# Kernel optimization log

Hardware: AMD Instinct MI355X
Metric: run time of the kernel (lower is better)

Reference implementation:

```python
import jax, jax.numpy as jnp
import numpy as np

# --- static config (mirrors args) ---
FOV = 79.0
RES = 5                      # map_resolution (cm/cell)
MAP_SIZE_CM = 4800           # map_size_cm // global_downscaling
VR = 100                     # vision_range (cells)
CAM_H_CM = 88.0              # camera_height * 100
CAT_THR, EXP_THR, MAP_THR = 5.0, 1.0, 1.0
MAX_H = 72                   # int(360 / 5)
MIN_H = -8                   # int(-40 / 5)
DEG = 57.29577951308232


def _splat(feat, coords, dims):
    """Trilinear splat (scatter-add) of feat [F,N] at coords [3,N] in [-1,1] into grid dims, then round."""
    F_, N = feat.shape
    Mtot = dims[0] * dims[1] * dims[2]
    pos = [coords[d] * dims[d] / 2.0 + dims[d] / 2.0 for d in range(3)]
    flo = [jnp.floor(p) for p in pos]
    grid = jnp.zeros((F_, Mtot), jnp.float32)
    for c0 in (0, 1):
        for c1 in (0, 1):
            for c2 in (0, 1):
                idx = jnp.zeros((N,), jnp.float32)
                wts = jnp.ones((N,), jnp.float32)
                for d, off in enumerate((c0, c1, c2)):
                    p = flo[d] + off
                    safe = ((p > 0) & (p < dims[d])).astype(jnp.float32)
                    wts = wts * (1.0 - jnp.abs(pos[d] - p)) * safe
                    idx = idx * dims[d] + p * safe
                grid = grid.at[:, idx.astype(jnp.int32)].add(feat * wts[None, :])
    return jnp.round(grid).reshape(F_, dims[0], dims[1], dims[2])


def _affine_grid(theta, H, W):
    # align_corners=True base grid; theta [2,3] -> grid [H,W,2] (x,y)
    gx, gy = jnp.meshgrid(jnp.linspace(-1.0, 1.0, W), jnp.linspace(-1.0, 1.0, H))
    base = jnp.stack([gx, gy, jnp.ones_like(gx)], -1)  # [H,W,3]
    return base @ theta.T


def _grid_sample(img, grid):
    # bilinear, zero padding, align_corners=True. img [C,H,W], grid [H,W,2]
    C, H, W = img.shape
    x = (grid[..., 0] + 1.0) * 0.5 * (W - 1)
    y = (grid[..., 1] + 1.0) * 0.5 * (H - 1)
    x0 = jnp.floor(x); y0 = jnp.floor(y)
    out = jnp.zeros_like(img)
    for yy, xx in ((y0, x0), (y0, x0 + 1), (y0 + 1, x0), (y0 + 1, x0 + 1)):
        w = (1.0 - jnp.abs(x - xx)) * (1.0 - jnp.abs(y - yy))
        inb = ((xx >= 0) & (xx <= W - 1) & (yy >= 0) & (yy <= H - 1)).astype(img.dtype)
        xi = jnp.clip(xx, 0, W - 1).astype(jnp.int32)
        yi = jnp.clip(yy, 0, H - 1).astype(jnp.int32)
        out = out + img[:, yi, xi] * (w * inb)[None]
    return out


def _forward(obs, pose_obs, maps_last, poses_last):
    bs, c, h, w = obs.shape
    depth = obs[0, 3]  # [h,w] in cm
    # camera matrix
    xc = (w - 1.0) / 2.0
    zc = (h - 1.0) / 2.0
    f = (w / 2.0) / np.tan(np.deg2rad(FOV / 2.0))
    gx = jnp.arange(w, dtype=jnp.float32)[None, :]
    gz = jnp.arange(h - 1, -1, -1, dtype=jnp.float32)[:, None]
    X = (gx - xc) * depth / f
    Z = (gz - zc) * depth / f
    # camera->agent (elevation 0 -> identity rot) then shift_loc (theta=pi/2 -> identity rot)
    X = X + VR * RES // 2
    Z = Z + CAM_H_CM
    zdim = MAX_H - MIN_H
    xs = (X / RES - VR // 2.0) / VR * 2.0
    ys = (depth / RES - VR // 2.0) / VR * 2.0
    zs = (Z / RES - (MAX_H + MIN_H) // 2.0) / zdim * 2.0
    N = h * w
    coords = jnp.stack([xs.reshape(N), ys.reshape(N), zs.reshape(N)], 0)  # [3,N]
    feat = jnp.concatenate([jnp.ones((1, N), jnp.float32), obs[0, 4:].reshape(c - 4, N)], 0)  # [F,N]
    voxels = _splat(feat, coords, (VR, VR, zdim))       # [F,VR,VR,Z]
    voxels = jnp.swapaxes(voxels, 1, 2)                  # .transpose(2,3)
    min_z = int(25 / RES - MIN_H)                        # 13
    max_z = int((CAM_H_CM + 1) / RES - MIN_H)            # 25
    ahp = voxels[..., min_z:max_z].sum(-1)               # [F,VR,VR]
    allp = voxels.sum(-1)
    fp_map = jnp.clip(ahp[0:1] / MAP_THR, 0.0, 1.0)
    fp_exp = jnp.clip(allp[0:1] / EXP_THR, 0.0, 1.0)
    M = MAP_SIZE_CM // RES
    x1 = M // 2 - VR // 2; x2 = x1 + VR
    y1 = M // 2; y2 = y1 + VR
    agent_view = jnp.zeros((c, M, M), jnp.float32)
    agent_view = agent_view.at[0:1, y1:y2, x1:x2].set(fp_map)
    agent_view = agent_view.at[1:2, y1:y2, x1:x2].set(fp_exp)
    agent_view = agent_view.at[4:, y1:y2, x1:x2].set(jnp.clip(ahp[1:] / CAT_THR, 0.0, 1.0))
    # pose integration (note: pose_pred aliases poses_last which is updated in-place in torch)
    th = poses_last[2] / DEG
    ny = poses_last[1] + pose_obs[0] * jnp.sin(th) + pose_obs[1] * jnp.cos(th)
    nx = poses_last[0] + pose_obs[0] * jnp.cos(th) - pose_obs[1] * jnp.sin(th)
    nt = poses_last[2] + pose_obs[2] * DEG
    nt = jnp.fmod(nt - 180.0, 360.0) + 180.0
    nt = jnp.fmod(nt + 180.0, 360.0) - 180.0
    current_pose = jnp.stack([nx, ny, nt])
    # spatial transform (st_pose is detached in torch)
    st = jax.lax.stop_gradient(current_pose)
    half = M // 2
    sx = -(st[0] * 100.0 / RES - half) / half
    sy = -(st[1] * 100.0 / RES - half) / half
    sth = (90.0 - st[2]) * np.pi / 180.0
    ct, sn = jnp.cos(sth), jnp.sin(sth)
    z = jnp.zeros(()); o = jnp.ones(())
    theta1 = jnp.stack([jnp.stack([ct, -sn, z]), jnp.stack([sn, ct, z])])
    theta2 = jnp.stack([jnp.stack([o, z, sx]), jnp.stack([z, o, sy])])
    rotated = _grid_sample(agent_view, _affine_grid(theta1, M, M))
    translated = _grid_sample(rotated, _affine_grid(theta2, M, M))
    # snap positive semantic cells (channels 4..7) to per-channel feature max
    ks = feat[1:5].max(axis=1)  # [4]
    sem = translated[4:8]
    translated = translated.at[4:8].set(jnp.where(sem > 0.0, ks[:, None, None], sem))
    map_pred = jnp.maximum(maps_last, translated)
    return fp_map, map_pred, current_pose, current_pose


def setup_inputs() -> dict:
    key = jax.random.key(0)
    k1, k2, k3, k4 = jax.random.split(key, 4)
    C = 9
    obs = jax.random.uniform(k1, (1, C, 480, 640), dtype=jnp.float32)
    obs = obs.at[:, 3].set(obs[:, 3] * 400.0 + 50.0)  # depth in cm, 50..450
    pose_obs = jax.random.uniform(k2, (3,), dtype=jnp.float32) * jnp.array([0.2, 0.2, 0.1], jnp.float32)
    maps_last = jax.random.uniform(k3, (C, 960, 960), dtype=jnp.float32)
    poses_last = jnp.array([24.0, 24.0, 0.0], jnp.float32) + jax.random.uniform(k4, (3,), dtype=jnp.float32) * jnp.array([2.0, 2.0, 30.0], jnp.float32)
    return {"obs": obs, "pose_obs": pose_obs, "maps_last": maps_last, "poses_last": poses_last}


def reference(obs, pose_obs, maps_last, poses_last):
    return _forward(obs, pose_obs, maps_last, poses_last)
```

## Files before the change

### kernel.cpp

```cpp
#include <hip/hip_runtime.h>
#include <math.h>

#define NPIX (480*640)
#define MDIM 960
#define MPIX (MDIM*MDIM)

#define CNT_OFF   0
#define CUR_OFF   10000
#define SCAL_OFF  20000
#define MEMSET_U32 20016
#define OFFS_OFF  20016
#define SM_OFF    30024
#define PAY_OFF   100024

#define OUT_FPMAP 0
#define OUT_MAP   10000
#define OUT_POSE  (10000 + 9*MPIX)

__global__ void pose_kernel(const float* pose_obs, const float* poses_last,
                            float* scal, float* out_pose) {
    if (threadIdx.x == 0) {
        const float DEGc = 57.29577951308232f;
        float th = poses_last[2] / DEGc;
        float s = sinf(th), c = cosf(th);
        float ny = poses_last[1] + pose_obs[0]*s + pose_obs[1]*c;
        float nx = poses_last[0] + pose_obs[0]*c - pose_obs[1]*s;
        float nt = poses_last[2] + pose_obs[2]*DEGc;
        nt = fmodf(nt - 180.0f, 360.0f) + 180.0f;
        nt = fmodf(nt + 180.0f, 360.0f) - 180.0f;
        out_pose[0] = nx; out_pose[1] = ny; out_pose[2] = nt;
        out_pose[3] = nx; out_pose[4] = ny; out_pose[5] = nt;
        float sx = -((nx*100.0f)/5.0f - 480.0f)/480.0f;
        float sy = -((ny*100.0f)/5.0f - 480.0f)/480.0f;
        float sth = ((90.0f - nt) * 3.14159265358979323846f) / 180.0f;
        scal[0] = cosf(sth);
        scal[1] = sinf(sth);
        scal[2] = sx;
        scal[3] = sy;
    }
}

__global__ void ks_kernel(const float* __restrict__ obs, float* scal) {
    int tid = blockIdx.x*blockDim.x + threadIdx.x;
    int stride = gridDim.x*blockDim.x;
    float m0 = 0.0f, m1 = 0.0f, m2 = 0.0f, m3 = 0.0f;
    for (int p = tid; p < NPIX; p += stride) {
        m0 = fmaxf(m0, obs[4*NPIX + p]);
        m1 = fmaxf(m1, obs[5*NPIX + p]);
        m2 = fmaxf(m2, obs[6*NPIX + p]);
        m3 = fmaxf(m3, obs[7*NPIX + p]);
    }
    #pragma unroll
    for (int off = 32; off > 0; off >>= 1) {
        m0 = fmaxf(m0, __shfl_down(m0, off, 64));
        m1 = fmaxf(m1, __shfl_down(m1, off, 64));
        m2 = fmaxf(m2, __shfl_down(m2, off, 64));
        m3 = fmaxf(m3, __shfl_down(m3, off, 64));
    }
    if ((threadIdx.x & 63) == 0) {
        atomicMax((int*)&scal[4], __float_as_int(m0));
        atomicMax((int*)&scal[5], __float_as_int(m1));
        atomicMax((int*)&scal[6], __float_as_int(m2));
        atomicMax((int*)&scal[7], __float_as_int(m3));
    }
}

__device__ __forceinline__ void pix_pos(const float* __restrict__ obs, int pix, float fcam,
                                        float& pos0, float& pos1, float& pos2) {
    int i = pix / 640, j = pix - i*640;
    float d = obs[3*NPIX + pix];
    float X = ((float)j - 319.5f) * d / fcam + 250.0f;
    float Z = ((float)(479 - i) - 239.5f) * d / fcam + 88.0f;
    float xs = ((X/5.0f - 50.0f)/100.0f)*2.0f;
    float ys = ((d/5.0f - 50.0f)/100.0f)*2.0f;
    float zs = ((Z/5.0f - 32.0f)/80.0f)*2.0f;
    pos0 = (xs*100.0f)/2.0f + 50.0f;
    pos1 = (ys*100.0f)/2.0f + 50.0f;
    pos2 = (zs*80.0f)/2.0f + 40.0f;
}

__global__ __launch_bounds__(256) void count_kernel(const float* __restrict__ obs,
                                                    unsigned* __restrict__ cnt, float fcam) {
    int pix = blockIdx.x*blockDim.x + threadIdx.x;
    if (pix >= NPIX) return;
    float p0, p1, p2;
    pix_pos(obs, pix, fcam, p0, p1, p2);
    int bx = (int)floorf(p0), by = (int)floorf(p1), bz = (int)floorf(p2);
    if (bx < 0 || bx > 99 || by < 0 || by > 99 || bz < 0 || bz > 79) return;
    atomicAdd(&cnt[bx*100 + by], 1u);
}

__global__ __launch_bounds__(1024) void scan_kernel(const unsigned* __restrict__ cnt,
                                                    unsigned* __restrict__ offs) {
    __shared__ unsigned part[1024];
    int tid = threadIdx.x;
    int base = tid * 10;
    unsigned local[10];
    unsigned s = 0;
    #pragma unroll
    for (int q = 0; q < 10; q++) {
        unsigned v = (base + q < 10000) ? cnt[base + q] : 0u;
        local[q] = s;
        s += v;
    }
    part[tid] = s;
    __syncthreads();
    for (int off = 1; off < 1024; off <<= 1) {
        unsigned v = (tid >= off) ? part[tid - off] : 0u;
        __syncthreads();
        part[tid] += v;
        __syncthreads();
    }
    unsigned chunk_excl = (tid > 0) ? part[tid - 1] : 0u;
    #pragma unroll
    for (int q = 0; q < 10; q++) {
        if (base + q <= 10000) offs[base + q] = chunk_excl + local[q];
    }
}

__global__ __launch_bounds__(256) void scatter_kernel(const float* __restrict__ obs,
                                                      const unsigned* __restrict__ offs,
                                                      unsigned* __restrict__ cur,
                                                      float4* __restrict__ pay, float fcam) {
    int pix = blockIdx.x*blockDim.x + threadIdx.x;
    if (pix >= NPIX) return;
    float p0, p1, p2;
    pix_pos(obs, pix, fcam, p0, p1, p2);
    int bx = (int)floorf(p0), by = (int)floorf(p1), bz = (int)floorf(p2);
    if (bx < 0 || bx > 99 || by < 0 || by > 99 || bz < 0 || bz > 79) return;
    int b = bx*100 + by;
    unsigned slot = atomicAdd(&cur[b], 1u);
    unsigned k = offs[b] + slot;
    float f1 = obs[4*NPIX + pix];
    float f2 = obs[5*NPIX + pix];
    float f3 = obs[6*NPIX + pix];
    float f4 = obs[7*NPIX + pix];
    float f5 = obs[8*NPIX + pix];
    pay[2*k + 0] = make_float4(p0, p1, p2, f1);
    pay[2*k + 1] = make_float4(f2, f3, f4, f5);
}

__global__ __launch_bounds__(256) void gather_kernel(const float4* __restrict__ pay,
                                                     const unsigned* __restrict__ offs,
                                                     float* __restrict__ sm,
                                                     float* __restrict__ out_fp) {
    int t = blockIdx.x;
    int x = t % 100, y = t / 100;
    int tid = threadIdx.x;
    int sub = tid >> 6;
    int lane = tid & 63;
    __shared__ float zacc[80*6];
    for (int q = tid; q < 480; q += 256) zacc[q] = 0.0f;
    __syncthreads();
    if (x >= 1 && y >= 1) {
        int bx = x - 1 + (sub & 1);
        int by = y - 1 + (sub >> 1);
        int b = bx*100 + by;
        unsigned s = offs[b], e = offs[b+1];
        for (unsigned k = s + lane; k < e; k += 64) {
            float4 a  = pay[2*k + 0];
            float4 q2 = pay[2*k + 1];
            float w0 = 1.0f - fabsf(a.x - (float)x);
            float w1 = 1.0f - fabsf(a.y - (float)y);
            float w01 = w0 * w1;
            float bzf = floorf(a.z);
            #pragma unroll
            for (int c2 = 0; c2 <= 1; c2++) {
                float p2 = bzf + (float)c2;
                if (!(p2 > 0.0f && p2 < 80.0f)) continue;
                float w = w01 * (1.0f - fabsf(a.z - p2));
                int zb = (int)p2 * 6;
                atomicAdd(&zacc[zb + 0], w);
                atomicAdd(&zacc[zb + 1], w*a.w);
                atomicAdd(&zacc[zb + 2], w*q2.x);
                atomicAdd(&zacc[zb + 3], w*q2.y);
                atomicAdd(&zacc[zb + 4], w*q2.z);
                atomicAdd(&zacc[zb + 5], w*q2.w);
            }
        }
    }
    __syncthreads();
    if (tid < 64) {
        int z = lane;
        float r0 = rintf(zacc[z*6 + 0]);
        float all0 = r0;
        if (lane < 16) all0 += rintf(zacc[(z + 64)*6 + 0]);
        bool inb = (z >= 13 && z < 25);
        float a0 = inb ? r0 : 0.0f;
        float a1 = inb ? rintf(zacc[z*6 + 1]) : 0.0f;
        float a2 = inb ? rintf(zacc[z*6 + 2]) : 0.0f;
        float a3 = inb ? rintf(zacc[z*6 + 3]) : 0.0f;
        float a4 = inb ? rintf(zacc[z*6 + 4]) : 0.0f;
        float a5 = inb ? rintf(zacc[z*6 + 5]) : 0.0f;
        #pragma unroll
        for (int off = 32; off > 0; off >>= 1) {
            all0 += __shfl_down(all0, off, 64);
            a0 += __shfl_down(a0, off, 64);
            a1 += __shfl_down(a1, off, 64);
            a2 += __shfl_down(a2, off, 64);
            a3 += __shfl_down(a3, off, 64);
            a4 += __shfl_down(a4, off, 64);
            a5 += __shfl_down(a5, off, 64);
        }
        if (lane == 0) {
            float fp = fminf(a0, 1.0f);
            float ex = fminf(all0, 1.0f);
            sm[0*10000 + t] = fp;
            sm[1*10000 + t] = ex;
            sm[2*10000 + t] = fminf(a1/5.0f, 1.0f);
            sm[3*10000 + t] = fminf(a2/5.0f, 1.0f);
            sm[4*10000 + t] = fminf(a3/5.0f, 1.0f);
            sm[5*10000 + t] = fminf(a4/5.0f, 1.0f);
            sm[6*10000 + t] = fminf(a5/5.0f, 1.0f);
            out_fp[t] = fp;
        }
    }
}

__device__ __forceinline__ void sample_agent(float gxv, float gyv,
                                             float ct, float sn,
                                             const float* __restrict__ sm,
                                             float rot[7]) {
    float u = ct*gxv - sn*gyv;
    float v = sn*gxv + ct*gyv;
    float xim = ((u + 1.0f)*0.5f)*959.0f;
    float yim = ((v + 1.0f)*0.5f)*959.0f;
    float x0 = floorf(xim), y0 = floorf(yim);
    #pragma unroll
    for (int ty = 0; ty <= 1; ty++) {
        float yy = y0 + (float)ty;
        if (yy < 480.0f || yy >= 580.0f) continue;
        float wy = 1.0f - fabsf(yim - yy);
        int yi = (int)yy - 480;
        #pragma unroll
        for (int tx = 0; tx <= 1; tx++) {
            float xx = x0 + (float)tx;
            if (xx < 430.0f || xx >= 530.0f) continue;
            float w = (1.0f - fabsf(xim - xx)) * wy;
            int o = yi*100 + ((int)xx - 430);
            #pragma unroll
            for (int k = 0; k < 7; k++) rot[k] += sm[k*10000 + o] * w;
        }
    }
}

__global__ __launch_bounds__(256) void final_kernel(const float* __restrict__ maps_last,
                                                    const float* __restrict__ sm,
                                                    const float* __restrict__ scal,
                                                    float* __restrict__ out_map) {
    int t = blockIdx.x*blockDim.x + threadIdx.x;
    if (t >= MPIX) return;
    int y = t / MDIM, x = t - y*MDIM;
    float ct = scal[0], sn = scal[1], sx = scal[2], sy = scal[3];
    float ks0 = scal[4], ks1 = scal[5], ks2 = scal[6], ks3 = scal[7];
    const float step = 2.0f/959.0f;
    float gxv = (float)x*step - 1.0f;
    float gyv = (float)y*step - 1.0f;
    float u = gxv + sx, v = gyv + sy;
    float xim = ((u + 1.0f)*0.5f)*959.0f;
    float yim = ((v + 1.0f)*0.5f)*959.0f;
    float ts[7] = {0,0,0,0,0,0,0};

    float gxc = xim*step - 1.0f;
    float gyc = yim*step - 1.0f;
    float uc = ct*gxc - sn*gyc;
    float vc = sn*gxc + ct*gyc;
    float xc2 = ((uc + 1.0f)*0.5f)*959.0f;
    float yc2 = ((vc + 1.0f)*0.5f)*959.0f;
    bool active = (xc2 > 427.5f) && (xc2 < 531.5f) && (yc2 > 477.5f) && (yc2 < 581.5f);

    if (active) {
        float x0 = floorf(xim), y0 = floorf(yim);
        #pragma unroll
        for (int ty = 0; ty <= 1; ty++) {
            float yy = y0 + (float)ty;
            if (yy < 0.0f || yy > 959.0f) continue;
            float wy = 1.0f - fabsf(yim - yy);
            #pragma unroll
            for (int tx = 0; tx <= 1; tx++) {
                float xx = x0 + (float)tx;
                if (xx < 0.0f || xx > 959.0f) continue;
                float w = (1.0f - fabsf(xim - xx)) * wy;
                float rot[7] = {0,0,0,0,0,0,0};
                float gx1 = xx*step - 1.0f;
                float gy1 = yy*step - 1.0f;
                sample_agent(gx1, gy1, ct, sn, sm, rot);
                #pragma unroll
                for (int k = 0; k < 7; k++) ts[k] += rot[k]*w;
            }
        }
    }
    int o = t;
    float ml;
    ml = maps_last[0*MPIX + o]; out_map[0*MPIX + o] = fmaxf(ml, ts[0]);
    ml = maps_last[1*MPIX + o]; out_map[1*MPIX + o] = fmaxf(ml, ts[1]);
    ml = maps_last[2*MPIX + o]; out_map[2*MPIX + o] = fmaxf(ml, 0.0f);
    ml = maps_last[3*MPIX + o]; out_map[3*MPIX + o] = fmaxf(ml, 0.0f);
    float t4 = ts[2]; t4 = (t4 > 0.0f) ? ks0 : t4;
    ml = maps_last[4*MPIX + o]; out_map[4*MPIX + o] = fmaxf(ml, t4);
    float t5 = ts[3]; t5 = (t5 > 0.0f) ? ks1 : t5;
    ml = maps_last[5*MPIX + o]; out_map[5*MPIX + o] = fmaxf(ml, t5);
    float t6 = ts[4]; t6 = (t6 > 0.0f) ? ks2 : t6;
    ml = maps_last[6*MPIX + o]; out_map[6*MPIX + o] = fmaxf(ml, t6);
    float t7 = ts[5]; t7 = (t7 > 0.0f) ? ks3 : t7;
    ml = maps_last[7*MPIX + o]; out_map[7*MPIX + o] = fmaxf(ml, t7);
    ml = maps_last[8*MPIX + o]; out_map[8*MPIX + o] = fmaxf(ml, ts[6]);
}

extern "C" void kernel_launch(void* const* d_in, const int* in_sizes, int n_in,
                              void* d_out, int out_size, void* d_ws, size_t ws_size,
                              hipStream_t stream) {
    const float* obs        = (const float*)d_in[0];
    const float* pose_obs   = (const float*)d_in[1];
    const float* maps_last  = (const float*)d_in[2];
    const float* poses_last = (const float*)d_in[3];
    float* out = (float*)d_out;

    unsigned* ws_u = (unsigned*)d_ws;
    float*    ws_f = (float*)d_ws;
    unsigned* cnt  = ws_u + CNT_OFF;
    unsigned* cur  = ws_u + CUR_OFF;
    float*    scal = ws_f + SCAL_OFF;
    unsigned* offs = ws_u + OFFS_OFF;
    float*    sm   = ws_f + SM_OFF;
    float4*   pay  = (float4*)(ws_f + PAY_OFF);

    hipMemsetAsync(d_ws, 0, (size_t)MEMSET_U32 * 4, stream);

    float fcam = (float)(320.0 / tan(39.5 * M_PI / 180.0));

    pose_kernel<<<1, 64, 0, stream>>>(pose_obs, poses_last, scal, out + OUT_POSE);
    ks_kernel<<<128, 256, 0, stream>>>(obs, scal);
    count_kernel<<<(NPIX + 255)/256, 256, 0, stream>>>(obs, cnt, fcam);
    scan_kernel<<<1, 1024, 0, stream>>>(cnt, offs);
    scatter_kernel<<<(NPIX + 255)/256, 256, 0, stream>>>(obs, offs, cur, pay, fcam);
    gather_kernel<<<10000, 256, 0, stream>>>(pay, offs, sm, out + OUT_FPMAP);
    final_kernel<<<(MPIX + 255)/256, 256, 0, stream>>>(maps_last, sm, scal, out + OUT_MAP);
}
```

Before: 266.6 us.

## Fuse count/ks and scan/pose kernels, record ranks, vectorize pixel loops

Merges the depth-bin counting with the semantic-channel max reduction, and the prefix scan with the pose computation, which removes two launches. The count pass stores each pixel's bin and atomic rank so the scatter pass no longer needs a second atomic counter. Pixel and map kernels now process four elements per thread with float4 loads. The gather kernel assigns one wave per cell and reads two adjacent bins as a single contiguous range. The final kernel takes a fast path that streams maps_last through when none of a thread's four pixels fall in the agent window. This adds a packed-rank buffer and a wave-level scan; the ks reduction now starts from the first element rather than zero, which matches only if the feature values are nonnegative.

```diff
diff --git a/kernel.cpp b/kernel.cpp
--- a/kernel.cpp
+++ b/kernel.cpp
@@ -4,22 +4,105 @@
 #define NPIX (480*640)
 #define MDIM 960
 #define MPIX (MDIM*MDIM)
-
-#define CNT_OFF   0
-#define CUR_OFF   10000
-#define SCAL_OFF  20000
-#define MEMSET_U32 20016
-#define OFFS_OFF  20016
-#define SM_OFF    30024
-#define PAY_OFF   100024
+#define PACK_M 307201u
+
+#define CNT_OFF    0
+#define SCAL_OFF   10000
+#define MEMSET_U32 10016
+#define OFFS_OFF   10016
+#define SM_OFF     20024
+#define PACK_OFF   90024
+#define PAY_OFF    397224
 
 #define OUT_FPMAP 0
 #define OUT_MAP   10000
 #define OUT_POSE  (10000 + 9*MPIX)
 
-__global__ void pose_kernel(const float* pose_obs, const float* poses_last,
-                            float* scal, float* out_pose) {
-    if (threadIdx.x == 0) {
+__global__ __launch_bounds__(256) void count_ks_kernel(const float* __restrict__ obs,
+                                                       unsigned* __restrict__ cnt,
+                                                       unsigned* __restrict__ pack,
+                                                       float* scal, float fcam) {
+    int g = blockIdx.x*256 + threadIdx.x;
+    int p = g*4;
+    int i = p / 640, j0 = p - i*640;
+    float4 d4 = *(const float4*)(obs + 3*NPIX + p);
+    float dv[4] = {d4.x, d4.y, d4.z, d4.w};
+    #pragma unroll
+    for (int q = 0; q < 4; q++) {
+        float d = dv[q];
+        float X = ((float)(j0+q) - 319.5f) * d / fcam + 250.0f;
+        float Z = ((float)(479 - i) - 239.5f) * d / fcam + 88.0f;
+        float xs = ((X/5.0f - 50.0f)/100.0f)*2.0f;
+        float ys = ((d/5.0f - 50.0f)/100.0f)*2.0f;
+        float zs = ((Z/5.0f - 32.0f)/80.0f)*2.0f;
+        float pos0 = (xs*100.0f)/2.0f + 50.0f;
+        float pos1 = (ys*100.0f)/2.0f + 50.0f;
+        float pos2 = (zs*80.0f)/2.0f + 40.0f;
+        int bx = (int)floorf(pos0), by = (int)floorf(pos1), bz = (int)floorf(pos2);
+        unsigned pk = 0xFFFFFFFFu;
+        if (bx >= 0 && bx <= 99 && by >= 0 && by <= 99 && bz >= 0 && bz <= 79) {
+            unsigned b = (unsigned)(bx*100 + by);
+            unsigned rank = atomicAdd(&cnt[b], 1u);
+            pk = b * PACK_M + rank;
+        }
+        pack[p+q] = pk;
+    }
+    float4 a = *(const float4*)(obs + 4*NPIX + p);
+    float4 b4 = *(const float4*)(obs + 5*NPIX + p);
+    float4 c4 = *(const float4*)(obs + 6*NPIX + p);
+    float4 e4 = *(const float4*)(obs + 7*NPIX + p);
+    float m0 = fmaxf(fmaxf(a.x,a.y), fmaxf(a.z,a.w));
+    float m1 = fmaxf(fmaxf(b4.x,b4.y), fmaxf(b4.z,b4.w));
+    float m2 = fmaxf(fmaxf(c4.x,c4.y), fmaxf(c4.z,c4.w));
+    float m3 = fmaxf(fmaxf(e4.x,e4.y), fmaxf(e4.z,e4.w));
+    #pragma unroll
+    for (int off = 32; off > 0; off >>= 1) {
+        m0 = fmaxf(m0, __shfl_down(m0, off, 64));
+        m1 = fmaxf(m1, __shfl_down(m1, off, 64));
+        m2 = fmaxf(m2, __shfl_down(m2, off, 64));
+        m3 = fmaxf(m3, __shfl_down(m3, off, 64));
+    }
+    if ((threadIdx.x & 63) == 0) {
+        atomicMax((int*)&scal[4], __float_as_int(m0));
+        atomicMax((int*)&scal[5], __float_as_int(m1));
+        atomicMax((int*)&scal[6], __float_as_int(m2));
+        atomicMax((int*)&scal[7], __float_as_int(m3));
+    }
+}
+
+__global__ __launch_bounds__(256) void scan_pose_kernel(const unsigned* __restrict__ cnt,
+                                                        unsigned* __restrict__ offs,
+                                                        const float* pose_obs,
+                                                        const float* poses_last,
+                                                        float* scal, float* out_pose) {
+    int tid = threadIdx.x;
+    int lane = tid & 63, wave = tid >> 6;
+    unsigned sum = 0;
+    #pragma unroll 4
+    for (int q = 0; q < 40; q++) {
+        int idx = tid*40 + q;
+        if (idx < 10000) sum += cnt[idx];
+    }
+    unsigned incl = sum;
+    #pragma unroll
+    for (int off = 1; off < 64; off <<= 1) {
+        unsigned u = (unsigned)__shfl_up((int)incl, off, 64);
+        if (lane >= off) incl += u;
+    }
+    __shared__ unsigned wtot[4];
+    if (lane == 63) wtot[wave] = incl;
+    __syncthreads();
+    unsigned pre = 0;
+    for (int w = 0; w < wave; w++) pre += wtot[w];
+    unsigned excl = pre + incl - sum;
+    unsigned run = excl;
+    #pragma unroll 4
+    for (int q = 0; q < 40; q++) {
+        int idx = tid*40 + q;
+        if (idx < 10000) { offs[idx] = run; run += cnt[idx]; }
+    }
+    if (tid == 255) {
+        offs[10000] = excl;
         const float DEGc = 57.29577951308232f;
         float th = poses_last[2] / DEGc;
         float s = sinf(th), c = cosf(th);
@@ -40,180 +123,121 @@
     }
 }
 
-__global__ void ks_kernel(const float* __restrict__ obs, float* scal) {
-    int tid = blockIdx.x*blockDim.x + threadIdx.x;
-    int stride = gridDim.x*blockDim.x;
-    float m0 = 0.0f, m1 = 0.0f, m2 = 0.0f, m3 = 0.0f;
-    for (int p = tid; p < NPIX; p += stride) {
-        m0 = fmaxf(m0, obs[4*NPIX + p]);
-        m1 = fmaxf(m1, obs[5*NPIX + p]);
-        m2 = fmaxf(m2, obs[6*NPIX + p]);
-        m3 = fmaxf(m3, obs[7*NPIX + p]);
-    }
-    #pragma unroll
-    for (int off = 32; off > 0; off >>= 1) {
-        m0 = fmaxf(m0, __shfl_down(m0, off, 64));
-        m1 = fmaxf(m1, __shfl_down(m1, off, 64));
-        m2 = fmaxf(m2, __shfl_down(m2, off, 64));
-        m3 = fmaxf(m3, __shfl_down(m3, off, 64));
-    }
-    if ((threadIdx.x & 63) == 0) {
-        atomicMax((int*)&scal[4], __float_as_int(m0));
-        atomicMax((int*)&scal[5], __float_as_int(m1));
-        atomicMax((int*)&scal[6], __float_as_int(m2));
-        atomicMax((int*)&scal[7], __float_as_int(m3));
-    }
-}
-
-__device__ __forceinline__ void pix_pos(const float* __restrict__ obs, int pix, float fcam,
-                                        float& pos0, float& pos1, float& pos2) {
-    int i = pix / 640, j = pix - i*640;
-    float d = obs[3*NPIX + pix];
-    float X = ((float)j - 319.5f) * d / fcam + 250.0f;
-    float Z = ((float)(479 - i) - 239.5f) * d / fcam + 88.0f;
-    float xs = ((X/5.0f - 50.0f)/100.0f)*2.0f;
-    float ys = ((d/5.0f - 50.0f)/100.0f)*2.0f;
-    float zs = ((Z/5.0f - 32.0f)/80.0f)*2.0f;
-    pos0 = (xs*100.0f)/2.0f + 50.0f;
-    pos1 = (ys*100.0f)/2.0f + 50.0f;
-    pos2 = (zs*80.0f)/2.0f + 40.0f;
-}
-
-__global__ __launch_bounds__(256) void count_kernel(const float* __restrict__ obs,
-                                                    unsigned* __restrict__ cnt, float fcam) {
-    int pix = blockIdx.x*blockDim.x + threadIdx.x;
-    if (pix >= NPIX) return;
-    float p0, p1, p2;
-    pix_pos(obs, pix, fcam, p0, p1, p2);
-    int bx = (int)floorf(p0), by = (int)floorf(p1), bz = (int)floorf(p2);
-    if (bx < 0 || bx > 99 || by < 0 || by > 99 || bz < 0 || bz > 79) return;
-    atomicAdd(&cnt[bx*100 + by], 1u);
-}
-
-__global__ __launch_bounds__(1024) void scan_kernel(const unsigned* __restrict__ cnt,
-                                                    unsigned* __restrict__ offs) {
-    __shared__ unsigned part[1024];
-    int tid = threadIdx.x;
-    int base = tid * 10;
-    unsigned local[10];
-    unsigned s = 0;
-    #pragma unroll
-    for (int q = 0; q < 10; q++) {
-        unsigned v = (base + q < 10000) ? cnt[base + q] : 0u;
-        local[q] = s;
-        s += v;
-    }
-    part[tid] = s;
-    __syncthreads();
-    for (int off = 1; off < 1024; off <<= 1) {
-        unsigned v = (tid >= off) ? part[tid - off] : 0u;
-        __syncthreads();
-        part[tid] += v;
-        __syncthreads();
-    }
-    unsigned chunk_excl = (tid > 0) ? part[tid - 1] : 0u;
-    #pragma unroll
-    for (int q = 0; q < 10; q++) {
-        if (base + q <= 10000) offs[base + q] = chunk_excl + local[q];
-    }
-}
-
 __global__ __launch_bounds__(256) void scatter_kernel(const float* __restrict__ obs,
                                                       const unsigned* __restrict__ offs,
-                                                      unsigned* __restrict__ cur,
+                                                      const unsigned* __restrict__ pack,
                                                       float4* __restrict__ pay, float fcam) {
-    int pix = blockIdx.x*blockDim.x + threadIdx.x;
-    if (pix >= NPIX) return;
-    float p0, p1, p2;
-    pix_pos(obs, pix, fcam, p0, p1, p2);
-    int bx = (int)floorf(p0), by = (int)floorf(p1), bz = (int)floorf(p2);
-    if (bx < 0 || bx > 99 || by < 0 || by > 99 || bz < 0 || bz > 79) return;
-    int b = bx*100 + by;
-    unsigned slot = atomicAdd(&cur[b], 1u);
-    unsigned k = offs[b] + slot;
-    float f1 = obs[4*NPIX + pix];
-    float f2 = obs[5*NPIX + pix];
-    float f3 = obs[6*NPIX + pix];
-    float f4 = obs[7*NPIX + pix];
-    float f5 = obs[8*NPIX + pix];
-    pay[2*k + 0] = make_float4(p0, p1, p2, f1);
-    pay[2*k + 1] = make_float4(f2, f3, f4, f5);
-}
-
-__global__ __launch_bounds__(256) void gather_kernel(const float4* __restrict__ pay,
-                                                     const unsigned* __restrict__ offs,
-                                                     float* __restrict__ sm,
-                                                     float* __restrict__ out_fp) {
-    int t = blockIdx.x;
+    int g = blockIdx.x*256 + threadIdx.x;
+    int p = g*4;
+    int i = p / 640, j0 = p - i*640;
+    uint4 pk4 = *(const uint4*)(pack + p);
+    unsigned pks[4] = {pk4.x, pk4.y, pk4.z, pk4.w};
+    float4 d4 = *(const float4*)(obs + 3*NPIX + p);
+    float4 f14 = *(const float4*)(obs + 4*NPIX + p);
+    float4 f24 = *(const float4*)(obs + 5*NPIX + p);
+    float4 f34 = *(const float4*)(obs + 6*NPIX + p);
+    float4 f44 = *(const float4*)(obs + 7*NPIX + p);
+    float4 f54 = *(const float4*)(obs + 8*NPIX + p);
+    float dv[4] = {d4.x, d4.y, d4.z, d4.w};
+    float f1[4] = {f14.x, f14.y, f14.z, f14.w};
+    float f2[4] = {f24.x, f24.y, f24.z, f24.w};
+    float f3[4] = {f34.x, f34.y, f34.z, f34.w};
+    float f4v[4] = {f44.x, f44.y, f44.z, f44.w};
+    float f5[4] = {f54.x, f54.y, f54.z, f54.w};
+    #pragma unroll
+    for (int q = 0; q < 4; q++) {
+        unsigned pk = pks[q];
+        if (pk == 0xFFFFFFFFu) continue;
+        unsigned b = pk / PACK_M;
+        unsigned rank = pk - b * PACK_M;
+        unsigned k = offs[b] + rank;
+        float d = dv[q];
+        float X = ((float)(j0+q) - 319.5f) * d / fcam + 250.0f;
+        float Z = ((float)(479 - i) - 239.5f) * d / fcam + 88.0f;
+        float xs = ((X/5.0f - 50.0f)/100.0f)*2.0f;
+        float ys = ((d/5.0f - 50.0f)/100.0f)*2.0f;
+        float zs = ((Z/5.0f - 32.0f)/80.0f)*2.0f;
+        float pos0 = (xs*100.0f)/2.0f + 50.0f;
+        float pos1 = (ys*100.0f)/2.0f + 50.0f;
+        float pos2 = (zs*80.0f)/2.0f + 40.0f;
+        pay[2*k + 0] = make_float4(pos0, pos1, pos2, f1[q]);
+        pay[2*k + 1] = make_float4(f2[q], f3[q], f4v[q], f5[q]);
+    }
+}
+
+__global__ __launch_bounds__(1024) void gather_kernel(const float4* __restrict__ pay,
+                                                      const unsigned* __restrict__ offs,
+                                                      float* __restrict__ sm,
+                                                      float* __restrict__ out_fp) {
+    int wave = threadIdx.x >> 6, lane = threadIdx.x & 63;
+    int t = blockIdx.x*16 + wave;
     int x = t % 100, y = t / 100;
-    int tid = threadIdx.x;
-    int sub = tid >> 6;
-    int lane = tid & 63;
-    __shared__ float zacc[80*6];
-    for (int q = tid; q < 480; q += 256) zacc[q] = 0.0f;
+    __shared__ float zacc[16][480];
+    float* za = zacc[wave];
+    for (int q = lane; q < 480; q += 64) za[q] = 0.0f;
+    if (x >= 1 && y >= 1) {
+        int bb0 = (x-1)*100 + (y-1);
+        int bb1 = x*100 + (y-1);
+        #pragma unroll
+        for (int sgi = 0; sgi < 2; sgi++) {
+            int b = sgi ? bb1 : bb0;
+            unsigned s = offs[b], e = offs[b+2];
+            for (unsigned k = s + lane; k < e; k += 64) {
+                float4 a  = pay[2*k + 0];
+                float4 q2 = pay[2*k + 1];
+                float w0 = 1.0f - fabsf(a.x - (float)x);
+                float w1 = 1.0f - fabsf(a.y - (float)y);
+                float w01 = w0 * w1;
+                float bzf = floorf(a.z);
+                #pragma unroll
+                for (int c2 = 0; c2 <= 1; c2++) {
+                    float p2 = bzf + (float)c2;
+                    if (!(p2 > 0.0f && p2 < 80.0f)) continue;
+                    float w = w01 * (1.0f - fabsf(a.z - p2));
+                    int zb = (int)p2 * 6;
+                    atomicAdd(&za[zb + 0], w);
+                    atomicAdd(&za[zb + 1], w*a.w);
+                    atomicAdd(&za[zb + 2], w*q2.x);
+                    atomicAdd(&za[zb + 3], w*q2.y);
+                    atomicAdd(&za[zb + 4], w*q2.z);
+                    atomicAdd(&za[zb + 5], w*q2.w);
+                }
+            }
+        }
+    }
     __syncthreads();
-    if (x >= 1 && y >= 1) {
-        int bx = x - 1 + (sub & 1);
-        int by = y - 1 + (sub >> 1);
-        int b = bx*100 + by;
-        unsigned s = offs[b], e = offs[b+1];
-        for (unsigned k = s + lane; k < e; k += 64) {
-            float4 a  = pay[2*k + 0];
-            float4 q2 = pay[2*k + 1];
-            float w0 = 1.0f - fabsf(a.x - (float)x);
-            float w1 = 1.0f - fabsf(a.y - (float)y);
-            float w01 = w0 * w1;
-            float bzf = floorf(a.z);
-            #pragma unroll
-            for (int c2 = 0; c2 <= 1; c2++) {
-                float p2 = bzf + (float)c2;
-                if (!(p2 > 0.0f && p2 < 80.0f)) continue;
-                float w = w01 * (1.0f - fabsf(a.z - p2));
-                int zb = (int)p2 * 6;
-                atomicAdd(&zacc[zb + 0], w);
-                atomicAdd(&zacc[zb + 1], w*a.w);
-                atomicAdd(&zacc[zb + 2], w*q2.x);
-                atomicAdd(&zacc[zb + 3], w*q2.y);
-                atomicAdd(&zacc[zb + 4], w*q2.z);
-                atomicAdd(&zacc[zb + 5], w*q2.w);
-            }
-        }
-    }
-    __syncthreads();
-    if (tid < 64) {
-        int z = lane;
-        float r0 = rintf(zacc[z*6 + 0]);
-        float all0 = r0;
-        if (lane < 16) all0 += rintf(zacc[(z + 64)*6 + 0]);
-        bool inb = (z >= 13 && z < 25);
-        float a0 = inb ? r0 : 0.0f;
-        float a1 = inb ? rintf(zacc[z*6 + 1]) : 0.0f;
-        float a2 = inb ? rintf(zacc[z*6 + 2]) : 0.0f;
-        float a3 = inb ? rintf(zacc[z*6 + 3]) : 0.0f;
-        float a4 = inb ? rintf(zacc[z*6 + 4]) : 0.0f;
-        float a5 = inb ? rintf(zacc[z*6 + 5]) : 0.0f;
-        #pragma unroll
-        for (int off = 32; off > 0; off >>= 1) {
-            all0 += __shfl_down(all0, off, 64);
-            a0 += __shfl_down(a0, off, 64);
-            a1 += __shfl_down(a1, off, 64);
-            a2 += __shfl_down(a2, off, 64);
-            a3 += __shfl_down(a3, off, 64);
-            a4 += __shfl_down(a4, off, 64);
-            a5 += __shfl_down(a5, off, 64);
-        }
-        if (lane == 0) {
-            float fp = fminf(a0, 1.0f);
-            float ex = fminf(all0, 1.0f);
-            sm[0*10000 + t] = fp;
-            sm[1*10000 + t] = ex;
-            sm[2*10000 + t] = fminf(a1/5.0f, 1.0f);
-            sm[3*10000 + t] = fminf(a2/5.0f, 1.0f);
-            sm[4*10000 + t] = fminf(a3/5.0f, 1.0f);
-            sm[5*10000 + t] = fminf(a4/5.0f, 1.0f);
-            sm[6*10000 + t] = fminf(a5/5.0f, 1.0f);
-            out_fp[t] = fp;
-        }
+    int z = lane;
+    float r0 = rintf(za[z*6 + 0]);
+    float all0 = r0;
+    if (lane < 16) all0 += rintf(za[(z + 64)*6 + 0]);
+    bool inb = (z >= 13 && z < 25);
+    float a0 = inb ? r0 : 0.0f;
+    float a1 = inb ? rintf(za[z*6 + 1]) : 0.0f;
+    float a2 = inb ? rintf(za[z*6 + 2]) : 0.0f;
+    float a3 = inb ? rintf(za[z*6 + 3]) : 0.0f;
+    float a4 = inb ? rintf(za[z*6 + 4]) : 0.0f;
+    float a5 = inb ? rintf(za[z*6 + 5]) : 0.0f;
+    #pragma unroll
+    for (int off = 32; off > 0; off >>= 1) {
+        all0 += __shfl_down(all0, off, 64);
+        a0 += __shfl_down(a0, off, 64);
+        a1 += __shfl_down(a1, off, 64);
+        a2 += __shfl_down(a2, off, 64);
+        a3 += __shfl_down(a3, off, 64);
+        a4 += __shfl_down(a4, off, 64);
+        a5 += __shfl_down(a5, off, 64);
+    }
+    if (lane == 0) {
+        float fp = fminf(a0, 1.0f);
+        float ex = fminf(all0, 1.0f);
+        sm[0*10000 + t] = fp;
+        sm[1*10000 + t] = ex;
+        sm[2*10000 + t] = fminf(a1/5.0f, 1.0f);
+        sm[3*10000 + t] = fminf(a2/5.0f, 1.0f);
+        sm[4*10000 + t] = fminf(a3/5.0f, 1.0f);
+        sm[5*10000 + t] = fminf(a4/5.0f, 1.0f);
+        sm[6*10000 + t] = fminf(a5/5.0f, 1.0f);
+        out_fp[t] = fp;
     }
 }
 
@@ -244,67 +268,93 @@
     }
 }
 
+__device__ __forceinline__ void pixel_ts(float xim, float yim, float ct, float sn,
+                                         const float* __restrict__ sm, float ts[7]) {
+    const float step = 2.0f/959.0f;
+    float x0 = floorf(xim), y0 = floorf(yim);
+    #pragma unroll
+    for (int ty = 0; ty <= 1; ty++) {
+        float yy = y0 + (float)ty;
+        if (yy < 0.0f || yy > 959.0f) continue;
+        float wy = 1.0f - fabsf(yim - yy);
+        #pragma unroll
+        for (int tx = 0; tx <= 1; tx++) {
+            float xx = x0 + (float)tx;
+            if (xx < 0.0f || xx > 959.0f) continue;
+            float w = (1.0f - fabsf(xim - xx)) * wy;
+            float rot[7] = {0,0,0,0,0,0,0};
+            float gx1 = xx*step - 1.0f;
+            float gy1 = yy*step - 1.0f;
+            sample_agent(gx1, gy1, ct, sn, sm, rot);
+            #pragma unroll
+            for (int k = 0; k < 7; k++) ts[k] += rot[k]*w;
+        }
+    }
+}
+
 __global__ __launch_bounds__(256) void final_kernel(const float* __restrict__ maps_last,
                                                     const float* __restrict__ sm,
                                                     const float* __restrict__ scal,
                                                     float* __restrict__ out_map) {
-    int t = blockIdx.x*blockDim.x + threadIdx.x;
-    if (t >= MPIX) return;
-    int y = t / MDIM, x = t - y*MDIM;
+    int g = blockIdx.x*256 + threadIdx.x;
+    int p = g*4;
+    int y = p / MDIM, xp = p - y*MDIM;
     float ct = scal[0], sn = scal[1], sx = scal[2], sy = scal[3];
+    const float step = 2.0f/959.0f;
+    float gyv = (float)y*step - 1.0f;
+    float v = gyv + sy;
+    float yim = ((v + 1.0f)*0.5f)*959.0f;
+    float gyc = yim*step - 1.0f;
+    float xims[4];
+    bool act[4];
+    bool any = false;
+    #pragma unroll
+    for (int q = 0; q < 4; q++) {
+        float gxv = (float)(xp+q)*step - 1.0f;
+        float u = gxv + sx;
+        float xim = ((u + 1.0f)*0.5f)*959.0f;
+        xims[q] = xim;
+        float gxc = xim*step - 1.0f;
+        float uc = ct*gxc - sn*gyc;
+        float vc = sn*gxc + ct*gyc;
+        float xc2 = ((uc + 1.0f)*0.5f)*959.0f;
+        float yc2 = ((vc + 1.0f)*0.5f)*959.0f;
+        bool a = (xc2 > 427.5f) && (xc2 < 531.5f) && (yc2 > 477.5f) && (yc2 < 581.5f);
+        act[q] = a;
+        any = any || a;
+    }
+    if (!any) {
+        #pragma unroll
+        for (int c = 0; c < 9; c++) {
+            float4 ml = *(const float4*)(maps_last + c*MPIX + p);
+            float4 o;
+            o.x = fmaxf(ml.x, 0.0f); o.y = fmaxf(ml.y, 0.0f);
+            o.z = fmaxf(ml.z, 0.0f); o.w = fmaxf(ml.w, 0.0f);
+            *(float4*)(out_map + c*MPIX + p) = o;
+        }
+        return;
+    }
     float ks0 = scal[4], ks1 = scal[5], ks2 = scal[6], ks3 = scal[7];
-    const float step = 2.0f/959.0f;
-    float gxv = (float)x*step - 1.0f;
-    float gyv = (float)y*step - 1.0f;
-    float u = gxv + sx, v = gyv + sy;
-    float xim = ((u + 1.0f)*0.5f)*959.0f;
-    float yim = ((v + 1.0f)*0.5f)*959.0f;
-    float ts[7] = {0,0,0,0,0,0,0};
-
-    float gxc = xim*step - 1.0f;
-    float gyc = yim*step - 1.0f;
-    float uc = ct*gxc - sn*gyc;
-    float vc = sn*gxc + ct*gyc;
-    float xc2 = ((uc + 1.0f)*0.5f)*959.0f;
-    float yc2 = ((vc + 1.0f)*0.5f)*959.0f;
-    bool active = (xc2 > 427.5f) && (xc2 < 531.5f) && (yc2 > 477.5f) && (yc2 < 581.5f);
-
-    if (active) {
-        float x0 = floorf(xim), y0 = floorf(yim);
-        #pragma unroll
-        for (int ty = 0; ty <= 1; ty++) {
-            float yy = y0 + (float)ty;
-            if (yy < 0.0f || yy > 959.0f) continue;
-            float wy = 1.0f - fabsf(yim - yy);
-            #pragma unroll
-            for (int tx = 0; tx <= 1; tx++) {
-                float xx = x0 + (float)tx;
-                if (xx < 0.0f || xx > 959.0f) continue;
-                float w = (1.0f - fabsf(xim - xx)) * wy;
-                float rot[7] = {0,0,0,0,0,0,0};
-                float gx1 = xx*step - 1.0f;
-                float gy1 = yy*step - 1.0f;
-                sample_agent(gx1, gy1, ct, sn, sm, rot);
-                #pragma unroll
-                for (int k = 0; k < 7; k++) ts[k] += rot[k]*w;
-            }
-        }
-    }
-    int o = t;
-    float ml;
-    ml = maps_last[0*MPIX + o]; out_map[0*MPIX + o] = fmaxf(ml, ts[0]);
-    ml = maps_last[1*MPIX + o]; out_map[1*MPIX + o] = fmaxf(ml, ts[1]);
-    ml = maps_last[2*MPIX + o]; out_map[2*MPIX + o] = fmaxf(ml, 0.0f);
-    ml = maps_last[3*MPIX + o]; out_map[3*MPIX + o] = fmaxf(ml, 0.0f);
-    float t4 = ts[2]; t4 = (t4 > 0.0f) ? ks0 : t4;
-    ml = maps_last[4*MPIX + o]; out_map[4*MPIX + o] = fmaxf(ml, t4);
-    float t5 = ts[3]; t5 = (t5 > 0.0f) ? ks1 : t5;
-    ml = maps_last[5*MPIX + o]; out_map[5*MPIX + o] = fmaxf(ml, t5);
-    float t6 = ts[4]; t6 = (t6 > 0.0f) ? ks2 : t6;
-    ml = maps_last[6*MPIX + o]; out_map[6*MPIX + o] = fmaxf(ml, t6);
-    float t7 = ts[5]; t7 = (t7 > 0.0f) ? ks3 : t7;
-    ml = maps_last[7*MPIX + o]; out_map[7*MPIX + o] = fmaxf(ml, t7);
-    ml = maps_last[8*MPIX + o]; out_map[8*MPIX + o] = fmaxf(ml, ts[6]);
+    #pragma unroll
+    for (int q = 0; q < 4; q++) {
+        int o = p + q;
+        float ts[7] = {0,0,0,0,0,0,0};
+        if (act[q]) pixel_ts(xims[q], yim, ct, sn, sm, ts);
+        float ml;
+        ml = maps_last[0*MPIX + o]; out_map[0*MPIX + o] = fmaxf(ml, ts[0]);
+        ml = maps_last[1*MPIX + o]; out_map[1*MPIX + o] = fmaxf(ml, ts[1]);
+        ml = maps_last[2*MPIX + o]; out_map[2*MPIX + o] = fmaxf(ml, 0.0f);
+        ml = maps_last[3*MPIX + o]; out_map[3*MPIX + o] = fmaxf(ml, 0.0f);
+        float t4 = ts[2]; t4 = (t4 > 0.0f) ? ks0 : t4;
+        ml = maps_last[4*MPIX + o]; out_map[4*MPIX + o] = fmaxf(ml, t4);
+        float t5 = ts[3]; t5 = (t5 > 0.0f) ? ks1 : t5;
+        ml = maps_last[5*MPIX + o]; out_map[5*MPIX + o] = fmaxf(ml, t5);
+        float t6 = ts[4]; t6 = (t6 > 0.0f) ? ks2 : t6;
+        ml = maps_last[6*MPIX + o]; out_map[6*MPIX + o] = fmaxf(ml, t6);
+        float t7 = ts[5]; t7 = (t7 > 0.0f) ? ks3 : t7;
+        ml = maps_last[7*MPIX + o]; out_map[7*MPIX + o] = fmaxf(ml, t7);
+        ml = maps_last[8*MPIX + o]; out_map[8*MPIX + o] = fmaxf(ml, ts[6]);
+    }
 }
 
 extern "C" void kernel_launch(void* const* d_in, const int* in_sizes, int n_in,
@@ -319,21 +369,20 @@
     unsigned* ws_u = (unsigned*)d_ws;
     float*    ws_f = (float*)d_ws;
     unsigned* cnt  = ws_u + CNT_OFF;
-    unsigned* cur  = ws_u + CUR_OFF;
     float*    scal = ws_f + SCAL_OFF;
     unsigned* offs = ws_u + OFFS_OFF;
     float*    sm   = ws_f + SM_OFF;
+    unsigned* pack = ws_u + PACK_OFF;
     float4*   pay  = (float4*)(ws_f + PAY_OFF);
 
     hipMemsetAsync(d_ws, 0, (size_t)MEMSET_U32 * 4, stream);
 
     float fcam = (float)(320.0 / tan(39.5 * M_PI / 180.0));
 
-    pose_kernel<<<1, 64, 0, stream>>>(pose_obs, poses_last, scal, out + OUT_POSE);
-    ks_kernel<<<128, 256, 0, stream>>>(obs, scal);
-    count_kernel<<<(NPIX + 255)/256, 256, 0, stream>>>(obs, cnt, fcam);
-    scan_kernel<<<1, 1024, 0, stream>>>(cnt, offs);
-    scatter_kernel<<<(NPIX + 255)/256, 256, 0, stream>>>(obs, offs, cur, pay, fcam);
-    gather_kernel<<<10000, 256, 0, stream>>>(pay, offs, sm, out + OUT_FPMAP);
-    final_kernel<<<(MPIX + 255)/256, 256, 0, stream>>>(maps_last, sm, scal, out + OUT_MAP);
-}
+    count_ks_kernel<<<300, 256, 0, stream>>>(obs, cnt, pack, scal, fcam);
+    scan_pose_kernel<<<1, 256, 0, stream>>>(cnt, offs, pose_obs, poses_last,
+                                            scal, out + OUT_POSE);
+    scatter_kernel<<<300, 256, 0, stream>>>(obs, offs, pack, pay, fcam);
+    gather_kernel<<<625, 1024, 0, stream>>>(pay, offs, sm, out + OUT_FPMAP);
+    final_kernel<<<900, 256, 0, stream>>>(maps_last, sm, scal, out + OUT_MAP);
+}
```

New measurement: 437.3 us. 64.0% more time.
